# Kernel tuning notes

Measured on AMD Instinct MI355X. Metric: run time of the kernel, lower is better.

The kernel has to match this reference:

```python
import jax, jax.numpy as jnp
import numpy as np

BS, SEQ, HID = 2, 2048, 1024
HEADS, BLOCK = 16, 64
HEAD_DIM = HID // HEADS


def setup_inputs() -> dict:
    key = jax.random.key(0)
    ks = jax.random.split(key, 5)
    s = 1.0 / np.sqrt(HID)
    return {
        "hidden_states": jax.random.normal(ks[0], (BS, SEQ, HID), jnp.float32),
        "Wq": jax.random.normal(ks[1], (HID, HID), jnp.float32) * s,
        "bq": jnp.zeros((HID,), jnp.float32),
        "Wk": jax.random.normal(ks[2], (HID, HID), jnp.float32) * s,
        "bk": jnp.zeros((HID,), jnp.float32),
        "Wv": jax.random.normal(ks[3], (HID, HID), jnp.float32) * s,
        "bv": jnp.zeros((HID,), jnp.float32),
        "Wo": jax.random.normal(ks[4], (HID, HID), jnp.float32) * s,
        "bo": jnp.zeros((HID,), jnp.float32),
    }


def reference(hidden_states, Wq, bq, Wk, bk, Wv, bv, Wo, bo):
    b, s, _ = hidden_states.shape
    # torch Linear: y = x @ W.T + b
    q = (hidden_states @ Wq.T + bq).reshape(b, s, HEADS, HEAD_DIM)
    k = (hidden_states @ Wk.T + bk).reshape(b, s, HEADS, HEAD_DIM)
    v = (hidden_states @ Wv.T + bv).reshape(b, s, HEADS, HEAD_DIM)
    scale = 1.0 / np.sqrt(HEAD_DIM).astype(np.float32)
    scores = jnp.einsum("bqhd,bkhd->bhqk", q, k) * scale  # [B,H,S,S]
    # block-level causal mask: kv block index <= query block index
    blk = jnp.arange(s) // BLOCK
    mask = blk[None, :] <= blk[:, None]  # [S,S]
    scores = jnp.where(mask[None, None], scores, jnp.finfo(scores.dtype).min)
    attn = jax.nn.softmax(scores, axis=-1)
    out = jnp.einsum("bhqk,bkhd->bqhd", attn, v).reshape(b, s, HID)
    return out @ Wo.T + bo
```

## Files before the change

### kernel.cpp

```cpp
#include <hip/hip_runtime.h>

#define BS 2
#define SEQ 2048
#define HID 1024
#define HEADS 16
#define HDIM 64
#define MTOT (BS * SEQ)

typedef __bf16 bf16x8 __attribute__((ext_vector_type(8)));
typedef float floatx4 __attribute__((ext_vector_type(4)));
typedef short short8 __attribute__((ext_vector_type(8)));
typedef unsigned short u16x4 __attribute__((ext_vector_type(4)));
typedef unsigned int u32x2 __attribute__((ext_vector_type(2)));

__device__ __forceinline__ floatx4 mfma16x16x32bf16(short8 a, short8 b, floatx4 c) {
    return __builtin_amdgcn_mfma_f32_16x16x32_bf16(
        __builtin_bit_cast(bf16x8, a), __builtin_bit_cast(bf16x8, b), c, 0, 0, 0);
}

__device__ __forceinline__ unsigned short f2bf(float f) {
    unsigned int u = __builtin_bit_cast(unsigned int, f);
    u += 0x7fffu + ((u >> 16) & 1u);
    return (unsigned short)(u >> 16);
}

#define GLOAD_LDS16(gsrc, ldst)                                                   \
    __builtin_amdgcn_global_load_lds(                                             \
        (const __attribute__((address_space(1))) void*)(gsrc),                    \
        (__attribute__((address_space(3))) void*)(ldst), 16, 0, 0)

__global__ __launch_bounds__(256) void cvt5(
    const float* __restrict__ X, const float* __restrict__ Wq,
    const float* __restrict__ Wk, const float* __restrict__ Wv,
    const float* __restrict__ Wo, unsigned short* __restrict__ dst)
{
    const int y = blockIdx.y;
    const float* src = (y == 0) ? X : (y == 1) ? Wq : (y == 2) ? Wk : (y == 3) ? Wv : Wo;
    const size_t base = (y == 0) ? 0 : (size_t)(4u << 20) + (size_t)(y - 1) * (1u << 20);
    const int n4 = (y == 0) ? (1 << 20) : (1 << 18);
    const float scale = (y == 1) ? 0.125f : 1.0f;
    int i = blockIdx.x * 256 + threadIdx.x;
    if (i >= n4) return;
    floatx4 v = *(const floatx4*)(src + (size_t)i * 4);
    v *= scale;
    unsigned int p0 = (unsigned int)f2bf(v[0]) | ((unsigned int)f2bf(v[1]) << 16);
    unsigned int p1 = (unsigned int)f2bf(v[2]) | ((unsigned int)f2bf(v[3]) << 16);
    u32x2 pk = {p0, p1};
    *(u32x2*)(dst + base + (size_t)i * 4) = pk;
}

template <int BM, int BN, int MODE>
__global__ __launch_bounds__(256) void gemm_bt(
    const unsigned short* __restrict__ X,
    const unsigned short* __restrict__ W0, const unsigned short* __restrict__ W1,
    const unsigned short* __restrict__ W2,
    const float* __restrict__ B0, const float* __restrict__ B1,
    const float* __restrict__ B2,
    unsigned short* __restrict__ out_bf, float* __restrict__ out_f)
{
    constexpr int MT = BM / 32, NT = BN / 32;
    constexpr int NCH = (BM + BN) * 4;
    __shared__ __align__(16) unsigned short sA[BM * 32];
    __shared__ __align__(16) unsigned short sB[BN * 32];

    const int tid  = threadIdx.x;
    const int z    = (MODE == 1) ? blockIdx.z : 0;
    const unsigned short* W  = (z == 0) ? W0 : (z == 1) ? W1 : W2;
    const float*          Bb = (z == 0) ? B0 : (z == 1) ? B1 : B2;
    const float bscale = (MODE == 1 && z == 0) ? 0.125f : 1.0f;
    const int m0   = blockIdx.x * BM;
    const int n0   = blockIdx.y * BN;
    const int lane = tid & 63, w = tid >> 6;
    const int l16  = lane & 15, grp = lane >> 4;
    const int wm   = w & 1, wn = w >> 1;

    floatx4 acc[MT][NT];
#pragma unroll
    for (int i = 0; i < MT; ++i)
#pragma unroll
        for (int j = 0; j < NT; ++j) acc[i][j] = (floatx4){0.f, 0.f, 0.f, 0.f};

    auto stage = [&](int kb) {
        const int kcol = kb * 32;
#pragma unroll
        for (int i = 0; i < NCH / 256; ++i) {
            int g = tid + i * 256;
            if (g < BM * 4) {
                int row = g >> 2, c8 = (g & 3) * 8;
                GLOAD_LDS16(X + (size_t)(m0 + row) * HID + kcol + c8, &sA[g * 8]);
            } else {
                int g2 = g - BM * 4;
                int row = g2 >> 2, c8 = (g2 & 3) * 8;
                GLOAD_LDS16(W + (size_t)(n0 + row) * HID + kcol + c8, &sB[g2 * 8]);
            }
        }
    };

    const bool swapT = (MODE == 1) && (z < 2);
    stage(0);
    for (int kb = 0; kb < 32; ++kb) {
        __syncthreads();
        short8 af[MT], bfr[NT];
#pragma unroll
        for (int t = 0; t < MT; ++t)
            af[t] = *(const short8*)&sA[(wm * (BM / 2) + t * 16 + l16) * 32 + grp * 8];
#pragma unroll
        for (int t = 0; t < NT; ++t)
            bfr[t] = *(const short8*)&sB[(wn * (BN / 2) + t * 16 + l16) * 32 + grp * 8];
        __syncthreads();
        if (kb + 1 < 32) stage(kb + 1);
        if (swapT) {
#pragma unroll
            for (int mt = 0; mt < MT; ++mt)
#pragma unroll
                for (int nt = 0; nt < NT; ++nt)
                    acc[mt][nt] = mfma16x16x32bf16(bfr[nt], af[mt], acc[mt][nt]);
        } else {
#pragma unroll
            for (int mt = 0; mt < MT; ++mt)
#pragma unroll
                for (int nt = 0; nt < NT; ++nt)
                    acc[mt][nt] = mfma16x16x32bf16(af[mt], bfr[nt], acc[mt][nt]);
        }
    }

    if (MODE == 0) {
#pragma unroll
        for (int nt = 0; nt < NT; ++nt) {
            int n = n0 + wn * (BN / 2) + nt * 16 + l16;
            float bias = Bb[n];
#pragma unroll
            for (int mt = 0; mt < MT; ++mt)
#pragma unroll
                for (int r = 0; r < 4; ++r) {
                    int m = m0 + wm * (BM / 2) + mt * 16 + grp * 4 + r;
                    out_f[(size_t)m * HID + n] = acc[mt][nt][r] + bias;
                }
        }
    } else if (z == 0) {
        const int hidx = (n0 + wn * 64) >> 6;
#pragma unroll
        for (int nt = 0; nt < NT; ++nt) {
            int dbase = nt * 16 + grp * 4;
            floatx4 b4 = *(const floatx4*)&Bb[n0 + wn * 64 + dbase];
            b4 *= bscale;
#pragma unroll
            for (int mt = 0; mt < MT; ++mt) {
                int m = m0 + wm * 32 + mt * 16 + l16;
                int bidx = m >> 11, s = m & (SEQ - 1);
                u16x4 pk;
#pragma unroll
                for (int r = 0; r < 4; ++r) pk[r] = f2bf(acc[mt][nt][r] + b4[r]);
                *(u16x4*)&out_bf[
                    ((((size_t)bidx * HEADS + hidx) * SEQ + s) * HDIM + dbase)] = pk;
            }
        }
    } else if (z == 1) {
        const size_t outz = (size_t)MTOT * HID;
        const int hidx = (n0 + wn * 64) >> 6;
        const int bidx = m0 >> 11;
        const int kvb  = (m0 & (SEQ - 1)) >> 6;
        const size_t hbase = outz + ((size_t)bidx * HEADS + hidx) * SEQ * HDIM;
        const int grpf = grp >> 1, j0 = (grp & 1) * 4;
#pragma unroll
        for (int nt = 0; nt < NT; ++nt) {
            floatx4 b4 = *(const floatx4*)&Bb[n0 + wn * 64 + nt * 16 + grp * 4];
#pragma unroll
            for (int mt = 0; mt < MT; ++mt) {
                u16x4 pk;
#pragma unroll
                for (int r = 0; r < 4; ++r) pk[r] = f2bf(acc[mt][nt][r] + b4[r]);
                size_t F = hbase
                    + (size_t)((((kvb * 4 + (wm * 2 + mt)) * 2 + (nt >> 1)) * 512)
                    + ((((nt & 1) * 2 + grpf) * 16 + l16) * 8) + j0);
                *(u16x4*)&out_bf[F] = pk;
            }
        }
    } else {
        const size_t outz = (size_t)2 * ((size_t)MTOT * HID);
        const int hidx = (n0 + wn * 64) >> 6;
        const int bidx = m0 >> 11;
        const int kvb  = (m0 & (SEQ - 1)) >> 6;
        const size_t hbase = outz + ((size_t)bidx * HEADS + hidx) * SEQ * HDIM;
        const int j0 = (grp & 1) * 4;
#pragma unroll
        for (int nt = 0; nt < NT; ++nt) {
            float bias = Bb[n0 + wn * 64 + nt * 16 + l16];
#pragma unroll
            for (int mt = 0; mt < MT; ++mt) {
                u16x4 pk;
#pragma unroll
                for (int r = 0; r < 4; ++r) pk[r] = f2bf(acc[mt][nt][r] + bias);
                size_t F = hbase + (size_t)((((kvb * 4 + nt) * 2 + wm) * 512)
                    + (((mt * 2 + (grp >> 1)) * 16 + l16) * 8) + j0);
                *(u16x4*)&out_bf[F] = pk;
            }
        }
    }
}

__global__ __launch_bounds__(64) void attn_kernel(
    const unsigned short* __restrict__ Qw, const unsigned short* __restrict__ Kf,
    const unsigned short* __restrict__ Vf, unsigned short* __restrict__ X2)
{
    __shared__ __align__(16) unsigned short Ps[16][72];

    const int id = blockIdx.x;
    const int xcd = id & 7, k = id >> 3;
    const int bh  = (k >> 6) * 8 + xcd;
    const int slot = k & 63;
    const int pairj = slot >> 2;
    const int quarter = slot & 3;
    const int b = bh >> 4, h = bh & 15;

    const int lane = threadIdx.x & 63;
    const int l16  = lane & 15, grp = lane >> 4;

    const size_t head = ((size_t)b * HEADS + h) * (size_t)SEQ * HDIM;
    const unsigned short* Kh = Kf + head;
    const unsigned short* Vh = Vf + head;

    short8 ka[4][2], kbuf[4][2], vf[4][2];

    auto loadK = [&](short8 (&kf)[4][2], int kb) {
#pragma unroll
        for (int nt = 0; nt < 4; ++nt)
#pragma unroll
            for (int ks = 0; ks < 2; ++ks)
                kf[nt][ks] = *(const short8*)(Kh +
                    (size_t)(((kb * 4 + nt) * 2 + ks) * 512) + lane * 8);
    };

#pragma unroll 1
    for (int phase = 0; phase < 2; ++phase) {
        const int qblk = phase ? (31 - pairj) : pairj;
        const int nkb  = qblk + 1;
        const int q0   = qblk * 64 + quarter * 16;

        short8 qf[2];
#pragma unroll
        for (int ks = 0; ks < 2; ++ks)
            qf[ks] = *(const short8*)(Qw + head +
                (size_t)(q0 + l16) * HDIM + ks * 32 + grp * 8);

        floatx4 o[4];
#pragma unroll
        for (int i = 0; i < 4; ++i) o[i] = (floatx4){0.f, 0.f, 0.f, 0.f};
        float mi = -1e30f, li = 0.f;

        auto process = [&](short8 (&kfc)[4][2], short8 (&kfn)[4][2], int kb) {
            {
#pragma unroll
                for (int nt = 0; nt < 4; ++nt)
#pragma unroll
                    for (int ks = 0; ks < 2; ++ks)
                        vf[nt][ks] = *(const short8*)(Vh +
                            (size_t)(((kb * 4 + nt) * 2 + ks) * 512) + lane * 8);
            }
            floatx4 sv[4];
#pragma unroll
            for (int nt = 0; nt < 4; ++nt) {
                floatx4 zz = (floatx4){0.f, 0.f, 0.f, 0.f};
                zz = mfma16x16x32bf16(kfc[nt][0], qf[0], zz);
                zz = mfma16x16x32bf16(kfc[nt][1], qf[1], zz);
                sv[nt] = zz;
            }
            if (kb + 1 < nkb) loadK(kfn, kb + 1);

            float m01 = fmaxf(fmaxf(sv[0][0], sv[0][1]), fmaxf(sv[0][2], sv[0][3]));
            float m23 = fmaxf(fmaxf(sv[1][0], sv[1][1]), fmaxf(sv[1][2], sv[1][3]));
            float m45 = fmaxf(fmaxf(sv[2][0], sv[2][1]), fmaxf(sv[2][2], sv[2][3]));
            float m67 = fmaxf(fmaxf(sv[3][0], sv[3][1]), fmaxf(sv[3][2], sv[3][3]));
            float mx = fmaxf(fmaxf(m01, m23), fmaxf(m45, m67));
            mx = fmaxf(mx, __shfl_xor(mx, 16));
            mx = fmaxf(mx, __shfl_xor(mx, 32));
            float mn = fmaxf(mi, mx);
            float alpha = __expf(mi - mn);
            mi = mn;
            float rs = 0.f;
#pragma unroll
            for (int nt = 0; nt < 4; ++nt) {
                floatx4 p;
#pragma unroll
                for (int r = 0; r < 4; ++r) p[r] = __expf(sv[nt][r] - mn);
                sv[nt] = p;
                rs += (p[0] + p[1]) + (p[2] + p[3]);
            }
            rs += __shfl_xor(rs, 16);
            rs += __shfl_xor(rs, 32);
            li = li * alpha + rs;

#pragma unroll
            for (int nt = 0; nt < 4; ++nt) {
                u16x4 pk;
#pragma unroll
                for (int r = 0; r < 4; ++r) pk[r] = f2bf(sv[nt][r]);
                *(u16x4*)&Ps[l16][nt * 16 + grp * 4] = pk;
            }
#pragma unroll
            for (int dt = 0; dt < 4; ++dt) o[dt] *= alpha;

            short8 pf0 = *(const short8*)&Ps[l16][grp * 8];
            short8 pf1 = *(const short8*)&Ps[l16][32 + grp * 8];
#pragma unroll
            for (int dt = 0; dt < 4; ++dt) {
                o[dt] = mfma16x16x32bf16(vf[dt][0], pf0, o[dt]);
                o[dt] = mfma16x16x32bf16(vf[dt][1], pf1, o[dt]);
            }
        };

        loadK(ka, 0);
        int kb = 0;
        while (true) {
            process(ka, kbuf, kb);
            if (++kb >= nkb) break;
            process(kbuf, ka, kb);
            if (++kb >= nkb) break;
        }

        float inv = 1.0f / li;
        int srow = q0 + l16;
#pragma unroll
        for (int dt = 0; dt < 4; ++dt) {
            u16x4 pk;
#pragma unroll
            for (int r = 0; r < 4; ++r) pk[r] = f2bf(o[dt][r] * inv);
            *(u16x4*)&X2[((size_t)b * SEQ + srow) * HID +
                         h * HDIM + dt * 16 + grp * 4] = pk;
        }
    }
}

extern "C" void kernel_launch(void* const* d_in, const int* in_sizes, int n_in,
                              void* d_out, int out_size, void* d_ws, size_t ws_size,
                              hipStream_t stream) {
    int iX, iWq, ibq, iWk, ibk, iWv, ibv, iWo, ibo;
    if (in_sizes[0] == MTOT * HID) {
        iX = 0; iWq = 1; ibq = 2; iWk = 3; ibk = 4; iWv = 5; ibv = 6; iWo = 7; ibo = 8;
    } else {
        iWk = 0; iWo = 1; iWq = 2; iWv = 3; ibk = 4; ibo = 5; ibq = 6; ibv = 7; iX = 8;
    }
    const float* X  = (const float*)d_in[iX];
    const float* Wq = (const float*)d_in[iWq];
    const float* bq = (const float*)d_in[ibq];
    const float* Wk = (const float*)d_in[iWk];
    const float* bk = (const float*)d_in[ibk];
    const float* Wv = (const float*)d_in[iWv];
    const float* bv = (const float*)d_in[ibv];
    const float* Wo = (const float*)d_in[iWo];
    const float* bo = (const float*)d_in[ibo];
    float* out = (float*)d_out;

    unsigned short* ws = (unsigned short*)d_ws;
    const size_t T = (size_t)MTOT * HID;
    unsigned short* qw  = ws;
    unsigned short* kfr = ws + T;
    unsigned short* vfr = ws + 2 * T;
    unsigned short* x2  = ws + 3 * T;
    unsigned short* Xb  = ws + 4 * T;
    unsigned short* Wqb = Xb + T;
    unsigned short* Wkb = Wqb + (size_t)HID * HID;
    unsigned short* Wvb = Wkb + (size_t)HID * HID;
    unsigned short* Wob = Wvb + (size_t)HID * HID;

    cvt5<<<dim3(4096, 5), 256, 0, stream>>>(X, Wq, Wk, Wv, Wo, Xb);
    gemm_bt<64, 128, 1><<<dim3(64, 8, 3), 256, 0, stream>>>(
        Xb, Wqb, Wkb, Wvb, bq, bk, bv, qw, nullptr);
    attn_kernel<<<dim3(2048), 64, 0, stream>>>(qw, kfr, vfr, x2);
    gemm_bt<64, 64, 0><<<dim3(64, 16, 1), 256, 0, stream>>>(
        x2, Wob, Wob, Wob, bo, bo, bo, nullptr, out);
}
```

Baseline: 195.4 us.

## Fuse Q/K/V projections into one kernel sharing the X tile; widen output GEMM tile

The QKV projection now runs as a single kernel in which each block loads one X tile and computes all three projections, instead of launching three separate z-slices that each reload X. This cuts global loads of X, but each block now holds three times the accumulators and larger shared memory, and the grid shrinks from 1536 to 512 blocks. The output projection tile is also widened from 64x64 to 64x128, halving its grid to 512 blocks. The change risks lower occupancy and higher register pressure.

```diff
diff --git a/kernel.cpp b/kernel.cpp
--- a/kernel.cpp
+++ b/kernel.cpp
@@ -49,14 +49,139 @@
     *(u32x2*)(dst + base + (size_t)i * 4) = pk;
 }
 
-template <int BM, int BN, int MODE>
-__global__ __launch_bounds__(256) void gemm_bt(
+__global__ __launch_bounds__(256) void gemm_qkv(
     const unsigned short* __restrict__ X,
     const unsigned short* __restrict__ W0, const unsigned short* __restrict__ W1,
     const unsigned short* __restrict__ W2,
     const float* __restrict__ B0, const float* __restrict__ B1,
     const float* __restrict__ B2,
-    unsigned short* __restrict__ out_bf, float* __restrict__ out_f)
+    unsigned short* __restrict__ out_bf)
+{
+    __shared__ __align__(16) unsigned short sA[64 * 32];
+    __shared__ __align__(16) unsigned short sB[3][128 * 32];
+
+    const int tid  = threadIdx.x;
+    const int m0   = blockIdx.x * 64;
+    const int n0   = blockIdx.y * 128;
+    const int lane = tid & 63, w = tid >> 6;
+    const int l16  = lane & 15, grp = lane >> 4;
+    const int wm   = w & 1, wn = w >> 1;
+
+    const unsigned short* Wz[3] = {W0, W1, W2};
+
+    floatx4 acc[3][2][4];
+#pragma unroll
+    for (int z = 0; z < 3; ++z)
+#pragma unroll
+        for (int i = 0; i < 2; ++i)
+#pragma unroll
+            for (int j = 0; j < 4; ++j) acc[z][i][j] = (floatx4){0.f, 0.f, 0.f, 0.f};
+
+    auto stage = [&](int kb) {
+        const int kcol = kb * 32;
+        {
+            int row = tid >> 2, c8 = (tid & 3) * 8;
+            GLOAD_LDS16(X + (size_t)(m0 + row) * HID + kcol + c8, &sA[tid * 8]);
+        }
+#pragma unroll
+        for (int i = 0; i < 6; ++i) {
+            int g2 = tid + i * 256;
+            int z = g2 >> 9, g3 = g2 & 511;
+            int row = g3 >> 2, c8 = (g3 & 3) * 8;
+            GLOAD_LDS16(Wz[z] + (size_t)(n0 + row) * HID + kcol + c8, &sB[z][g3 * 8]);
+        }
+    };
+
+    stage(0);
+    for (int kb = 0; kb < 32; ++kb) {
+        __syncthreads();
+        short8 af[2], bfr[3][4];
+#pragma unroll
+        for (int t = 0; t < 2; ++t)
+            af[t] = *(const short8*)&sA[(wm * 32 + t * 16 + l16) * 32 + grp * 8];
+#pragma unroll
+        for (int z = 0; z < 3; ++z)
+#pragma unroll
+            for (int t = 0; t < 4; ++t)
+                bfr[z][t] = *(const short8*)&sB[z][(wn * 64 + t * 16 + l16) * 32 + grp * 8];
+        __syncthreads();
+        if (kb + 1 < 32) stage(kb + 1);
+#pragma unroll
+        for (int mt = 0; mt < 2; ++mt)
+#pragma unroll
+            for (int nt = 0; nt < 4; ++nt) {
+                acc[0][mt][nt] = mfma16x16x32bf16(bfr[0][nt], af[mt], acc[0][mt][nt]);
+                acc[1][mt][nt] = mfma16x16x32bf16(bfr[1][nt], af[mt], acc[1][mt][nt]);
+                acc[2][mt][nt] = mfma16x16x32bf16(af[mt], bfr[2][nt], acc[2][mt][nt]);
+            }
+    }
+
+    const int hidx = (n0 + wn * 64) >> 6;
+    {
+#pragma unroll
+        for (int nt = 0; nt < 4; ++nt) {
+            int dbase = nt * 16 + grp * 4;
+            floatx4 b4 = *(const floatx4*)&B0[n0 + wn * 64 + dbase];
+            b4 *= 0.125f;
+#pragma unroll
+            for (int mt = 0; mt < 2; ++mt) {
+                int m = m0 + wm * 32 + mt * 16 + l16;
+                int bidx = m >> 11, s = m & (SEQ - 1);
+                u16x4 pk;
+#pragma unroll
+                for (int r = 0; r < 4; ++r) pk[r] = f2bf(acc[0][mt][nt][r] + b4[r]);
+                *(u16x4*)&out_bf[
+                    ((((size_t)bidx * HEADS + hidx) * SEQ + s) * HDIM + dbase)] = pk;
+            }
+        }
+    }
+    {
+        const size_t outz = (size_t)MTOT * HID;
+        const int bidx = m0 >> 11;
+        const int kvb  = (m0 & (SEQ - 1)) >> 6;
+        const size_t hbase = outz + ((size_t)bidx * HEADS + hidx) * SEQ * HDIM;
+        const int grpf = grp >> 1, j0 = (grp & 1) * 4;
+#pragma unroll
+        for (int nt = 0; nt < 4; ++nt) {
+            floatx4 b4 = *(const floatx4*)&B1[n0 + wn * 64 + nt * 16 + grp * 4];
+#pragma unroll
+            for (int mt = 0; mt < 2; ++mt) {
+                u16x4 pk;
+#pragma unroll
+                for (int r = 0; r < 4; ++r) pk[r] = f2bf(acc[1][mt][nt][r] + b4[r]);
+                size_t F = hbase
+                    + (size_t)((((kvb * 4 + (wm * 2 + mt)) * 2 + (nt >> 1)) * 512)
+                    + ((((nt & 1) * 2 + grpf) * 16 + l16) * 8) + j0);
+                *(u16x4*)&out_bf[F] = pk;
+            }
+        }
+    }
+    {
+        const size_t outz = (size_t)2 * ((size_t)MTOT * HID);
+        const int bidx = m0 >> 11;
+        const int kvb  = (m0 & (SEQ - 1)) >> 6;
+        const size_t hbase = outz + ((size_t)bidx * HEADS + hidx) * SEQ * HDIM;
+        const int j0 = (grp & 1) * 4;
+#pragma unroll
+        for (int nt = 0; nt < 4; ++nt) {
+            float bias = B2[n0 + wn * 64 + nt * 16 + l16];
+#pragma unroll
+            for (int mt = 0; mt < 2; ++mt) {
+                u16x4 pk;
+#pragma unroll
+                for (int r = 0; r < 4; ++r) pk[r] = f2bf(acc[2][mt][nt][r] + bias);
+                size_t F = hbase + (size_t)((((kvb * 4 + nt) * 2 + wm) * 512)
+                    + (((mt * 2 + (grp >> 1)) * 16 + l16) * 8) + j0);
+                *(u16x4*)&out_bf[F] = pk;
+            }
+        }
+    }
+}
+
+template <int BM, int BN>
+__global__ __launch_bounds__(256) void gemm_out(
+    const unsigned short* __restrict__ X, const unsigned short* __restrict__ W,
+    const float* __restrict__ Bb, float* __restrict__ out_f)
 {
     constexpr int MT = BM / 32, NT = BN / 32;
     constexpr int NCH = (BM + BN) * 4;
@@ -64,10 +189,6 @@
     __shared__ __align__(16) unsigned short sB[BN * 32];
 
     const int tid  = threadIdx.x;
-    const int z    = (MODE == 1) ? blockIdx.z : 0;
-    const unsigned short* W  = (z == 0) ? W0 : (z == 1) ? W1 : W2;
-    const float*          Bb = (z == 0) ? B0 : (z == 1) ? B1 : B2;
-    const float bscale = (MODE == 1 && z == 0) ? 0.125f : 1.0f;
     const int m0   = blockIdx.x * BM;
     const int n0   = blockIdx.y * BN;
     const int lane = tid & 63, w = tid >> 6;
@@ -96,7 +217,6 @@
         }
     };
 
-    const bool swapT = (MODE == 1) && (z < 2);
     stage(0);
     for (int kb = 0; kb < 32; ++kb) {
         __syncthreads();
@@ -109,93 +229,24 @@
             bfr[t] = *(const short8*)&sB[(wn * (BN / 2) + t * 16 + l16) * 32 + grp * 8];
         __syncthreads();
         if (kb + 1 < 32) stage(kb + 1);
-        if (swapT) {
-#pragma unroll
-            for (int mt = 0; mt < MT; ++mt)
-#pragma unroll
-                for (int nt = 0; nt < NT; ++nt)
-                    acc[mt][nt] = mfma16x16x32bf16(bfr[nt], af[mt], acc[mt][nt]);
-        } else {
-#pragma unroll
-            for (int mt = 0; mt < MT; ++mt)
-#pragma unroll
-                for (int nt = 0; nt < NT; ++nt)
-                    acc[mt][nt] = mfma16x16x32bf16(af[mt], bfr[nt], acc[mt][nt]);
-        }
-    }
-
-    if (MODE == 0) {
-#pragma unroll
-        for (int nt = 0; nt < NT; ++nt) {
-            int n = n0 + wn * (BN / 2) + nt * 16 + l16;
-            float bias = Bb[n];
-#pragma unroll
-            for (int mt = 0; mt < MT; ++mt)
-#pragma unroll
-                for (int r = 0; r < 4; ++r) {
-                    int m = m0 + wm * (BM / 2) + mt * 16 + grp * 4 + r;
-                    out_f[(size_t)m * HID + n] = acc[mt][nt][r] + bias;
-                }
-        }
-    } else if (z == 0) {
-        const int hidx = (n0 + wn * 64) >> 6;
-#pragma unroll
-        for (int nt = 0; nt < NT; ++nt) {
-            int dbase = nt * 16 + grp * 4;
-            floatx4 b4 = *(const floatx4*)&Bb[n0 + wn * 64 + dbase];
-            b4 *= bscale;
-#pragma unroll
-            for (int mt = 0; mt < MT; ++mt) {
-                int m = m0 + wm * 32 + mt * 16 + l16;
-                int bidx = m >> 11, s = m & (SEQ - 1);
-                u16x4 pk;
-#pragma unroll
-                for (int r = 0; r < 4; ++r) pk[r] = f2bf(acc[mt][nt][r] + b4[r]);
-                *(u16x4*)&out_bf[
-                    ((((size_t)bidx * HEADS + hidx) * SEQ + s) * HDIM + dbase)] = pk;
-            }
-        }
-    } else if (z == 1) {
-        const size_t outz = (size_t)MTOT * HID;
-        const int hidx = (n0 + wn * 64) >> 6;
-        const int bidx = m0 >> 11;
-        const int kvb  = (m0 & (SEQ - 1)) >> 6;
-        const size_t hbase = outz + ((size_t)bidx * HEADS + hidx) * SEQ * HDIM;
-        const int grpf = grp >> 1, j0 = (grp & 1) * 4;
-#pragma unroll
-        for (int nt = 0; nt < NT; ++nt) {
-            floatx4 b4 = *(const floatx4*)&Bb[n0 + wn * 64 + nt * 16 + grp * 4];
-#pragma unroll
-            for (int mt = 0; mt < MT; ++mt) {
-                u16x4 pk;
-#pragma unroll
-                for (int r = 0; r < 4; ++r) pk[r] = f2bf(acc[mt][nt][r] + b4[r]);
-                size_t F = hbase
-                    + (size_t)((((kvb * 4 + (wm * 2 + mt)) * 2 + (nt >> 1)) * 512)
-                    + ((((nt & 1) * 2 + grpf) * 16 + l16) * 8) + j0);
-                *(u16x4*)&out_bf[F] = pk;
-            }
-        }
-    } else {
-        const size_t outz = (size_t)2 * ((size_t)MTOT * HID);
-        const int hidx = (n0 + wn * 64) >> 6;
-        const int bidx = m0 >> 11;
-        const int kvb  = (m0 & (SEQ - 1)) >> 6;
-        const size_t hbase = outz + ((size_t)bidx * HEADS + hidx) * SEQ * HDIM;
-        const int j0 = (grp & 1) * 4;
-#pragma unroll
-        for (int nt = 0; nt < NT; ++nt) {
-            float bias = Bb[n0 + wn * 64 + nt * 16 + l16];
-#pragma unroll
-            for (int mt = 0; mt < MT; ++mt) {
-                u16x4 pk;
-#pragma unroll
-                for (int r = 0; r < 4; ++r) pk[r] = f2bf(acc[mt][nt][r] + bias);
-                size_t F = hbase + (size_t)((((kvb * 4 + nt) * 2 + wm) * 512)
-                    + (((mt * 2 + (grp >> 1)) * 16 + l16) * 8) + j0);
-                *(u16x4*)&out_bf[F] = pk;
-            }
-        }
+#pragma unroll
+        for (int mt = 0; mt < MT; ++mt)
+#pragma unroll
+            for (int nt = 0; nt < NT; ++nt)
+                acc[mt][nt] = mfma16x16x32bf16(af[mt], bfr[nt], acc[mt][nt]);
+    }
+
+#pragma unroll
+    for (int nt = 0; nt < NT; ++nt) {
+        int n = n0 + wn * (BN / 2) + nt * 16 + l16;
+        float bias = Bb[n];
+#pragma unroll
+        for (int mt = 0; mt < MT; ++mt)
+#pragma unroll
+            for (int r = 0; r < 4; ++r) {
+                int m = m0 + wm * (BM / 2) + mt * 16 + grp * 4 + r;
+                out_f[(size_t)m * HID + n] = acc[mt][nt][r] + bias;
+            }
     }
 }
 
@@ -364,9 +415,8 @@
     unsigned short* Wob = Wvb + (size_t)HID * HID;
 
     cvt5<<<dim3(4096, 5), 256, 0, stream>>>(X, Wq, Wk, Wv, Wo, Xb);
-    gemm_bt<64, 128, 1><<<dim3(64, 8, 3), 256, 0, stream>>>(
-        Xb, Wqb, Wkb, Wvb, bq, bk, bv, qw, nullptr);
+    gemm_qkv<<<dim3(64, 8), 256, 0, stream>>>(
+        Xb, Wqb, Wkb, Wvb, bq, bk, bv, qw);
     attn_kernel<<<dim3(2048), 64, 0, stream>>>(qw, kfr, vfr, x2);
-    gemm_bt<64, 64, 0><<<dim3(64, 16, 1), 256, 0, stream>>>(
-        x2, Wob, Wob, Wob, bo, bo, bo, nullptr, out);
-}
+    gemm_out<64, 128><<<dim3(64, 8), 256, 0, stream>>>(x2, Wob, bo, out);
+}
```

Result: no change. 192.8 us (-1.3%).
